# Optimization experiments

Measured on AMD Instinct MI355X. Metric: run time of the kernel, lower is better.

The kernel has to match this reference:

```python
import jax, jax.numpy as jnp
import numpy as np
from jax import lax

BS, NT, CH, K = 8, 128, 1024, 4
H = 512  # num_output_chanls // 2 per direction (bidirectional)
G = 4 * H  # gate dim, PyTorch order i,f,g,o


def setup_inputs() -> dict:
    key = jax.random.key(0)
    ks = jax.random.split(key, 9)
    s = 1.0 / np.sqrt(H)
    u = lambda k_, shape: jax.random.uniform(k_, shape, jnp.float32, -s, s)
    return {
        "inputs": jax.random.normal(ks[0], (BS, NT, CH, K), jnp.float32),
        "Wih_f": u(ks[1], (K, G, CH)),
        "Whh_f": u(ks[2], (K, G, H)),
        "bih_f": u(ks[3], (K, G)),
        "bhh_f": u(ks[4], (K, G)),
        "Wih_b": u(ks[5], (K, G, CH)),
        "Whh_b": u(ks[6], (K, G, H)),
        "bih_b": u(ks[7], (K, G)),
        "bhh_b": u(ks[8], (K, G)),
    }


def _lstm_dir(x_tbck, Wih, Whh, bih, bhh, reverse):
    # x_tbck: [nt, bs, ch, k]; weights batched over k heads.
    bs = x_tbck.shape[1]
    k, _, h = Whh.shape
    bias = bih + bhh  # [k, 4h]

    def step(carry, x_t):
        h_prev, c_prev = carry
        # detach_hidden_state=True: hidden state detached each step
        h_prev = lax.stop_gradient(h_prev)
        c_prev = lax.stop_gradient(c_prev)
        gates = (jnp.einsum('bck,kgc->bkg', x_t, Wih)
                 + jnp.einsum('bkh,kgh->bkg', h_prev, Whh)
                 + bias)  # [bs, k, 4h]
        i, f, g, o = jnp.split(gates, 4, axis=-1)
        c_new = jax.nn.sigmoid(f) * c_prev + jax.nn.sigmoid(i) * jnp.tanh(g)
        h_new = jax.nn.sigmoid(o) * jnp.tanh(c_new)
        return (h_new, c_new), h_new

    init = (jnp.zeros((bs, k, h), x_tbck.dtype), jnp.zeros((bs, k, h), x_tbck.dtype))
    _, hs = lax.scan(step, init, x_tbck, reverse=reverse)  # [nt, bs, k, h]
    return hs


def reference(inputs, Wih_f, Whh_f, bih_f, bhh_f, Wih_b, Whh_b, bih_b, bhh_b):
    # inputs: [bs, nt, ch, k] -> scan over time
    x = jnp.transpose(inputs, (1, 0, 2, 3))  # [nt, bs, ch, k]
    hs_f = _lstm_dir(x, Wih_f, Whh_f, bih_f, bhh_f, reverse=False)
    hs_b = _lstm_dir(x, Wih_b, Whh_b, bih_b, bhh_b, reverse=True)
    # [nt, bs, k, h] -> [bs, nt, h, k]; concat forward/backward on hidden dim
    hs_f = jnp.transpose(hs_f, (1, 0, 3, 2))
    hs_b = jnp.transpose(hs_b, (1, 0, 3, 2))
    return jnp.concatenate([hs_f, hs_b], axis=2)  # [bs, nt, 2h, k]
```

## Files before the change

kernel.cpp:

```cpp
#include <hip/hip_runtime.h>
#include <stdint.h>


typedef __attribute__((ext_vector_type(8))) short short8;
typedef __attribute__((ext_vector_type(4))) float floatx4;
typedef unsigned long long ull;

#define POISON 0x7FC07FC07FC07FC0ull

#define LDS_BARRIER()                                       \
  do {                                                      \
    asm volatile("s_waitcnt lgkmcnt(0)" ::: "memory");      \
    __builtin_amdgcn_s_barrier();                           \
  } while (0)

#define GLOAD_LDS16(g, l)                                        \
  __builtin_amdgcn_global_load_lds(                              \
      (const __attribute__((address_space(1))) void*)(g),        \
      (__attribute__((address_space(3))) void*)(l), 16, 0, 0)

__device__ __forceinline__ unsigned short f2bf(float f) {
  unsigned u = __float_as_uint(f);
  u = (u + 0x7fffu + ((u >> 16) & 1u)) >> 16;
  return (unsigned short)u;
}
__device__ __forceinline__ float sigm(float x) { return 1.0f / (1.0f + __expf(-x)); }
__device__ __forceinline__ float tanh_f(float x) {
  float ax = fabsf(x);
  float e = __expf(-2.0f * ax);
  float t = (1.0f - e) / (1.0f + e);
  return x < 0.0f ? -t : t;
}

__global__ __launch_bounds__(256) void prep_k(
    const float* __restrict__ x,
    const float* __restrict__ Wih_f, const float* __restrict__ Wih_b,
    const float* __restrict__ Whh_f, const float* __restrict__ Whh_b,
    unsigned short* __restrict__ Xp, unsigned short* __restrict__ Wihb,
    unsigned short* __restrict__ Whhb, ull* __restrict__ stateS) {
  size_t i = (size_t)blockIdx.x * 256 + threadIdx.x;
  if (i < 1048576) {
    int g = (int)i;
    int m = g >> 10, c = g & 1023;
    int t = m >> 3, b = m & 7;
    float4 v = *(const float4*)(x + ((size_t)((b * 128 + t) * 1024 + c)) * 4);
    Xp[g]           = f2bf(v.x);
    Xp[1048576 + g] = f2bf(v.y);
    Xp[2097152 + g] = f2bf(v.z);
    Xp[3145728 + g] = f2bf(v.w);
  } else if (i < 3145728) {
    size_t j = i - 1048576;
    float4 v = ((const float4*)Wih_f)[j];
    ushort4 o;
    o.x = f2bf(v.x); o.y = f2bf(v.y); o.z = f2bf(v.z); o.w = f2bf(v.w);
    ((ushort4*)Wihb)[j] = o;
  } else if (i < 5242880) {
    size_t j = i - 3145728;
    float4 v = ((const float4*)Wih_b)[j];
    ushort4 o;
    o.x = f2bf(v.x); o.y = f2bf(v.y); o.z = f2bf(v.z); o.w = f2bf(v.w);
    ((ushort4*)Wihb)[2097152 + j] = o;
  } else if (i < 6291456) {
    size_t j = i - 5242880;
    float4 v = ((const float4*)Whh_f)[j];
    ushort4 o;
    o.x = f2bf(v.x); o.y = f2bf(v.y); o.z = f2bf(v.z); o.w = f2bf(v.w);
    ((ushort4*)Whhb)[j] = o;
  } else if (i < 7340032) {
    size_t j = i - 6291456;
    float4 v = ((const float4*)Whh_b)[j];
    ushort4 o;
    o.x = f2bf(v.x); o.y = f2bf(v.y); o.z = f2bf(v.z); o.w = f2bf(v.w);
    ((ushort4*)Whhb)[1048576 + j] = o;
  } else {
    stateS[i - 7340032] = POISON;
  }
}

__global__ __launch_bounds__(256) void gemm_ih_k(
    const unsigned short* __restrict__ Xp, const unsigned short* __restrict__ Wb,
    const float* __restrict__ bihf, const float* __restrict__ bhhf,
    const float* __restrict__ bihb, const float* __restrict__ bhhb,
    float* __restrict__ ih) {
  const int bid = blockIdx.x;
  const int xcd = bid & 7;
  const int q   = bid >> 3;
  const int mt  = q & 7;
  const int p   = (q >> 3) * 8 + xcd;
  const int dk  = p >> 4;
  const int ntl = p & 15;
  const int kh = dk & 3;
  const int tid = threadIdx.x;
  const int L = tid & 63, w = tid >> 6;
  const int wm = w & 1, wn = w >> 1;
  const int quad = L >> 4, lo = L & 15;

  __shared__ unsigned short As[128 * 32];
  __shared__ unsigned short Bs[128 * 32];

  const unsigned short* Ab = Xp + (size_t)kh * 1048576 + (size_t)mt * 128 * 1024;
  const unsigned short* Bb = Wb + (size_t)dk * 2097152 + (size_t)ntl * 128 * 1024;

  floatx4 acc[4][4] = {};

  for (int kc = 0; kc < 32; ++kc) {
#pragma unroll
    for (int ph = 0; ph < 2; ++ph) {
      int c = ph * 256 + w * 64 + L;
      int ldsb = (ph * 256 + w * 64) * 8;
      GLOAD_LDS16(Ab + (size_t)(c >> 2) * 1024 + kc * 32 + (c & 3) * 8, As + ldsb);
      GLOAD_LDS16(Bb + (size_t)(c >> 2) * 1024 + kc * 32 + (c & 3) * 8, Bs + ldsb);
    }
    __syncthreads();
    short8 af[4], bf[4];
#pragma unroll
    for (int mi = 0; mi < 4; ++mi)
      af[mi] = *(const short8*)(As + (wm * 64 + mi * 16 + lo) * 32 + quad * 8);
#pragma unroll
    for (int ni = 0; ni < 4; ++ni)
      bf[ni] = *(const short8*)(Bs + (wn * 64 + ni * 16 + lo) * 32 + quad * 8);
#pragma unroll
    for (int mi = 0; mi < 4; ++mi)
#pragma unroll
      for (int ni = 0; ni < 4; ++ni)
        acc[mi][ni] = __builtin_amdgcn_mfma_f32_16x16x32_bf16(af[mi], bf[ni], acc[mi][ni], 0, 0, 0);
    __syncthreads();
  }

  const float* bihp = (dk < 4) ? bihf : bihb;
  const float* bhhp = (dk < 4) ? bhhf : bhhb;
#pragma unroll
  for (int ni = 0; ni < 4; ++ni) {
    int g = ntl * 128 + wn * 64 + ni * 16 + lo;
    float bv = bihp[kh * 2048 + g] + bhhp[kh * 2048 + g];
#pragma unroll
    for (int mi = 0; mi < 4; ++mi)
#pragma unroll
      for (int r = 0; r < 4; ++r) {
        int m = mt * 128 + wm * 64 + mi * 16 + quad * 4 + r;
        ih[((size_t)dk * 1024 + m) * 2048 + g] = acc[mi][ni][r] + bv;
      }
  }
}

__global__ __launch_bounds__(256) void lstm_rec_k(
    const float* __restrict__ ih, const unsigned short* __restrict__ whh,
    float* __restrict__ out, ull* __restrict__ stateS) {
  const int tid = threadIdx.x;
  const int L = tid & 63;
  const int w = tid >> 6;
  const int grp = blockIdx.x & 7;
  const int d = grp >> 2, kh = grp & 3;
  const int wg = blockIdx.x >> 3;
  const int j0 = wg * 32;
  const int quad = L >> 4, lo = L & 15;

  __shared__ unsigned short h_lds[16 * 520];
  __shared__ float gbuf[4][8][32];

  for (int i = tid; i < 16 * 520; i += 256) h_lds[i] = 0;

  short8 bfrag[2][16];
#pragma unroll
  for (int ni = 0; ni < 2; ++ni) {
    const unsigned short* wb =
        whh + ((size_t)grp * 2048 + (size_t)(w * 512 + j0 + ni * 16 + lo)) * 512 + quad * 8;
#pragma unroll
    for (int kk = 0; kk < 16; ++kk) bfrag[ni][kk] = *(const short8*)(wb + kk * 32);
  }

  const int pb = tid >> 5, pjj = tid & 31;
  float creg = 0.0f;

  float ihv[2][4];
  {
    int t0 = d ? 127 : 0;
#pragma unroll
    for (int ni = 0; ni < 2; ++ni) {
      const float* ihp =
          ih + ((size_t)grp * 1024 + (size_t)t0 * 8) * 2048 + (w * 512 + j0 + ni * 16 + lo);
#pragma unroll
      for (int r = 0; r < 4; ++r) {
        int b = quad * 4 + r;
        ihv[ni][r] = (b < 8) ? ihp[(size_t)b * 2048] : 0.0f;
      }
    }
  }

  const int srow = tid >> 5;
  const int scol = (tid & 31) * 16;

  for (int s = 0; s < 128; ++s) {
    const int t = d ? (127 - s) : s;

    float ihvN[2][4];
    if (s < 127) {
      int tn = d ? (126 - s) : (s + 1);
#pragma unroll
      for (int ni = 0; ni < 2; ++ni) {
        const float* ihp =
            ih + ((size_t)grp * 1024 + (size_t)tn * 8) * 2048 + (w * 512 + j0 + ni * 16 + lo);
#pragma unroll
        for (int r = 0; r < 4; ++r) {
          int b = quad * 4 + r;
          ihvN[ni][r] = (b < 8) ? ihp[(size_t)b * 2048] : 0.0f;
        }
      }
    } else {
#pragma unroll
      for (int ni = 0; ni < 2; ++ni)
#pragma unroll
        for (int r = 0; r < 4; ++r) ihvN[ni][r] = 0.0f;
    }

    if (s) {
      const ull* src = stateS + ((size_t)grp * 128 + s) * 1024 + tid * 4;
      ull v0, v1, v2, v3;
      do {
        v0 = __hip_atomic_load(src + 0, __ATOMIC_RELAXED, __HIP_MEMORY_SCOPE_AGENT);
        v1 = __hip_atomic_load(src + 1, __ATOMIC_RELAXED, __HIP_MEMORY_SCOPE_AGENT);
        v2 = __hip_atomic_load(src + 2, __ATOMIC_RELAXED, __HIP_MEMORY_SCOPE_AGENT);
        v3 = __hip_atomic_load(src + 3, __ATOMIC_RELAXED, __HIP_MEMORY_SCOPE_AGENT);
      } while (v0 == POISON || v1 == POISON || v2 == POISON || v3 == POISON);
      unsigned short* dl = h_lds + srow * 520 + scol;
      *(ull*)(dl + 0) = v0;
      *(ull*)(dl + 4) = v1;
      *(ull*)(dl + 8) = v2;
      *(ull*)(dl + 12) = v3;
    }
    LDS_BARRIER();

    floatx4 acc[2] = {};
    floatx4 acc2[2] = {};
    {
      const unsigned short* ar = h_lds + lo * 520 + quad * 8;
#pragma unroll
      for (int kk = 0; kk < 16; kk += 2) {
        short8 a0 = *(const short8*)(ar + kk * 32);
        short8 a1 = *(const short8*)(ar + (kk + 1) * 32);
#pragma unroll
        for (int ni = 0; ni < 2; ++ni) {
          acc[ni]  = __builtin_amdgcn_mfma_f32_16x16x32_bf16(a0, bfrag[ni][kk], acc[ni], 0, 0, 0);
          acc2[ni] = __builtin_amdgcn_mfma_f32_16x16x32_bf16(a1, bfrag[ni][kk + 1], acc2[ni], 0, 0, 0);
        }
      }
    }
#pragma unroll
    for (int ni = 0; ni < 2; ++ni)
#pragma unroll
      for (int r = 0; r < 4; ++r) {
        int b = quad * 4 + r;
        if (b < 8) gbuf[w][b][ni * 16 + lo] = acc[ni][r] + acc2[ni][r] + ihv[ni][r];
      }
    LDS_BARRIER();

    {
      float ig = gbuf[0][pb][pjj], fg = gbuf[1][pb][pjj];
      float gg = gbuf[2][pb][pjj], og = gbuf[3][pb][pjj];
      float cn = sigm(fg) * creg + sigm(ig) * tanh_f(gg);
      creg = cn;
      float h = sigm(og) * tanh_f(cn);

      if (s < 127) {
        unsigned hs = f2bf(h);
        int base = L & ~3;
        unsigned v0 = __shfl(hs, base + 0);
        unsigned v1 = __shfl(hs, base + 1);
        unsigned v2 = __shfl(hs, base + 2);
        unsigned v3 = __shfl(hs, base + 3);
        if ((L & 3) == 0) {
          ull wv = (ull)v0 | ((ull)v1 << 16) | ((ull)v2 << 32) | ((ull)v3 << 48);
          ull* dst = stateS + ((size_t)grp * 128 + (s + 1)) * 1024 + pb * 128 + ((j0 + pjj) >> 2);
          __hip_atomic_store(dst, wv, __ATOMIC_RELAXED, __HIP_MEMORY_SCOPE_AGENT);
        }
      }
      out[(((size_t)pb * 128 + t) * 1024 + d * 512 + j0 + pjj) * 4 + kh] = h;
    }

#pragma unroll
    for (int ni = 0; ni < 2; ++ni)
#pragma unroll
      for (int r = 0; r < 4; ++r) ihv[ni][r] = ihvN[ni][r];
  }
}

extern "C" void kernel_launch(void* const* d_in, const int* in_sizes, int n_in,
                              void* d_out, int out_size, void* d_ws, size_t ws_size,
                              hipStream_t stream) {
  (void)in_sizes; (void)n_in; (void)out_size; (void)ws_size;
  const float* x     = (const float*)d_in[0];
  const float* Wih_f = (const float*)d_in[1];
  const float* Whh_f = (const float*)d_in[2];
  const float* bih_f = (const float*)d_in[3];
  const float* bhh_f = (const float*)d_in[4];
  const float* Wih_b = (const float*)d_in[5];
  const float* Whh_b = (const float*)d_in[6];
  const float* bih_b = (const float*)d_in[7];
  const float* bhh_b = (const float*)d_in[8];
  float* out = (float*)d_out;
  char* ws = (char*)d_ws;

  ull* stateS          = (ull*)ws;
  float* ihg           = (float*)(ws + (8ull << 20));
  unsigned short* Xp   = (unsigned short*)(ws + (72ull << 20));
  unsigned short* Wihb = (unsigned short*)(ws + (80ull << 20));
  unsigned short* Whhb = (unsigned short*)(ws + (112ull << 20));

  prep_k<<<32768, 256, 0, stream>>>(x, Wih_f, Wih_b, Whh_f, Whh_b, Xp, Wihb, Whhb, stateS);
  gemm_ih_k<<<1024, 256, 0, stream>>>(Xp, Wihb, bih_f, bhh_f, bih_b, bhh_b, ihg);
  lstm_rec_k<<<128, 256, 0, stream>>>(ihg, Whhb, out, stateS);
}
```

Measured before the change: 418.9 us.

## Split input-GEMM: 256x256 tile kernel for first head, vectorize input bf16 pack

Vectorizes the input conversion in prep_k so each thread packs four channels and issues 16-byte loads and 8-byte stores, reducing the thread count. The input-projection GEMM for direction/head 0 is moved to a new 256x256-tile kernel that uses 512 threads, double-buffered direct-to-LDS loads and an XOR-swizzled layout. The remaining 7 direction/head slices stay on the existing 128x128 kernel. This likely aims at a dependency: the recurrence for the first slice could then start earlier or get better reuse. It adds a second GEMM launch, and the large tile yields only 32 blocks for that slice.

```diff
diff --git a/kernel.cpp b/kernel.cpp
--- a/kernel.cpp
+++ b/kernel.cpp
@@ -39,41 +39,49 @@
     unsigned short* __restrict__ Xp, unsigned short* __restrict__ Wihb,
     unsigned short* __restrict__ Whhb, ull* __restrict__ stateS) {
   size_t i = (size_t)blockIdx.x * 256 + threadIdx.x;
-  if (i < 1048576) {
-    int g = (int)i;
-    int m = g >> 10, c = g & 1023;
+  if (i < 262144) {
+    int m = (int)i >> 8, cb = (int)i & 255;
     int t = m >> 3, b = m & 7;
-    float4 v = *(const float4*)(x + ((size_t)((b * 128 + t) * 1024 + c)) * 4);
-    Xp[g]           = f2bf(v.x);
-    Xp[1048576 + g] = f2bf(v.y);
-    Xp[2097152 + g] = f2bf(v.z);
-    Xp[3145728 + g] = f2bf(v.w);
-  } else if (i < 3145728) {
-    size_t j = i - 1048576;
+    const float* xs = x + ((size_t)((b * 128 + t) * 1024 + cb * 4)) * 4;
+    float4 v0 = ((const float4*)xs)[0];
+    float4 v1 = ((const float4*)xs)[1];
+    float4 v2 = ((const float4*)xs)[2];
+    float4 v3 = ((const float4*)xs)[3];
+    int o = m * 1024 + cb * 4;
+    ushort4 o0 = {f2bf(v0.x), f2bf(v1.x), f2bf(v2.x), f2bf(v3.x)};
+    ushort4 o1 = {f2bf(v0.y), f2bf(v1.y), f2bf(v2.y), f2bf(v3.y)};
+    ushort4 o2 = {f2bf(v0.z), f2bf(v1.z), f2bf(v2.z), f2bf(v3.z)};
+    ushort4 o3 = {f2bf(v0.w), f2bf(v1.w), f2bf(v2.w), f2bf(v3.w)};
+    *(ushort4*)(Xp + o)           = o0;
+    *(ushort4*)(Xp + 1048576 + o) = o1;
+    *(ushort4*)(Xp + 2097152 + o) = o2;
+    *(ushort4*)(Xp + 3145728 + o) = o3;
+  } else if (i < 2359296) {
+    size_t j = i - 262144;
     float4 v = ((const float4*)Wih_f)[j];
     ushort4 o;
     o.x = f2bf(v.x); o.y = f2bf(v.y); o.z = f2bf(v.z); o.w = f2bf(v.w);
     ((ushort4*)Wihb)[j] = o;
-  } else if (i < 5242880) {
-    size_t j = i - 3145728;
+  } else if (i < 4456448) {
+    size_t j = i - 2359296;
     float4 v = ((const float4*)Wih_b)[j];
     ushort4 o;
     o.x = f2bf(v.x); o.y = f2bf(v.y); o.z = f2bf(v.z); o.w = f2bf(v.w);
     ((ushort4*)Wihb)[2097152 + j] = o;
-  } else if (i < 6291456) {
-    size_t j = i - 5242880;
+  } else if (i < 5505024) {
+    size_t j = i - 4456448;
     float4 v = ((const float4*)Whh_f)[j];
     ushort4 o;
     o.x = f2bf(v.x); o.y = f2bf(v.y); o.z = f2bf(v.z); o.w = f2bf(v.w);
     ((ushort4*)Whhb)[j] = o;
-  } else if (i < 7340032) {
-    size_t j = i - 6291456;
+  } else if (i < 6553600) {
+    size_t j = i - 5505024;
     float4 v = ((const float4*)Whh_b)[j];
     ushort4 o;
     o.x = f2bf(v.x); o.y = f2bf(v.y); o.z = f2bf(v.z); o.w = f2bf(v.w);
     ((ushort4*)Whhb)[1048576 + j] = o;
   } else {
-    stateS[i - 7340032] = POISON;
+    stateS[i - 6553600] = POISON;
   }
 }
 
@@ -87,7 +95,7 @@
   const int q   = bid >> 3;
   const int mt  = q & 7;
   const int p   = (q >> 3) * 8 + xcd;
-  const int dk  = p >> 4;
+  const int dk  = (p >> 4) + 1;
   const int ntl = p & 15;
   const int kh = dk & 3;
   const int tid = threadIdx.x;
@@ -141,6 +149,85 @@
         ih[((size_t)dk * 1024 + m) * 2048 + g] = acc[mi][ni][r] + bv;
       }
   }
+}
+
+__global__ __launch_bounds__(512, 2) void gemm256_k(
+    const unsigned short* __restrict__ Xp, const unsigned short* __restrict__ Wb,
+    const float* __restrict__ bihf, const float* __restrict__ bhhf,
+    float* __restrict__ ih) {
+  const int mt = blockIdx.x & 3;
+  const int nt = blockIdx.x >> 2;
+  const int tid = threadIdx.x;
+  const int L = tid & 63, w = tid >> 6;
+  const int wm = w >> 2, wn = w & 3;
+  const int quad = L >> 4, lo = L & 15;
+
+  __shared__ unsigned short smem[65536];
+
+  const unsigned short* Ab = Xp + (size_t)mt * 256 * 1024;
+  const unsigned short* Bb = Wb + (size_t)nt * 256 * 1024;
+
+  floatx4 acc[8][4] = {};
+
+#define STAGE256(t, buf)                                                     \
+  do {                                                                       \
+    unsigned short* SA = smem + (buf) * 32768;                               \
+    unsigned short* SB = SA + 16384;                                         \
+    _Pragma("unroll")                                                        \
+    for (int j = 0; j < 4; ++j) {                                            \
+      int c = j * 512 + tid;                                                 \
+      int row = c >> 3;                                                      \
+      int qs = (c & 7) ^ (row & 7);                                          \
+      int ldsb = (j * 512 + w * 64) * 8;     \
+      GLOAD_LDS16(Ab + (size_t)row * 1024 + (t) * 64 + qs * 8, SA + ldsb);   \
+      GLOAD_LDS16(Bb + (size_t)row * 1024 + (t) * 64 + qs * 8, SB + ldsb);   \
+    }                                                                        \
+  } while (0)
+
+  STAGE256(0, 0);
+  __syncthreads();
+
+  for (int t = 0; t < 16; ++t) {
+    if (t < 15) STAGE256(t + 1, (t + 1) & 1);
+    const unsigned short* SA = smem + (t & 1) * 32768;
+    const unsigned short* SB = SA + 16384;
+#pragma unroll
+    for (int kk = 0; kk < 2; ++kk) {
+      short8 af[8], bf[4];
+#pragma unroll
+      for (int mi = 0; mi < 8; ++mi) {
+        int row = wm * 128 + mi * 16 + lo;
+        int slot = (kk * 4 + quad) ^ (row & 7);
+        af[mi] = *(const short8*)(SA + row * 64 + slot * 8);
+      }
+#pragma unroll
+      for (int ni = 0; ni < 4; ++ni) {
+        int row = wn * 64 + ni * 16 + lo;
+        int slot = (kk * 4 + quad) ^ (row & 7);
+        bf[ni] = *(const short8*)(SB + row * 64 + slot * 8);
+      }
+#pragma unroll
+      for (int mi = 0; mi < 8; ++mi)
+#pragma unroll
+        for (int ni = 0; ni < 4; ++ni)
+          acc[mi][ni] = __builtin_amdgcn_mfma_f32_16x16x32_bf16(af[mi], bf[ni], acc[mi][ni], 0, 0, 0);
+    }
+    __syncthreads();
+  }
+
+#pragma unroll
+  for (int ni = 0; ni < 4; ++ni) {
+    int g = nt * 256 + wn * 64 + ni * 16 + lo;
+    float bv = bihf[g] + bhhf[g];
+#pragma unroll
+    for (int mi = 0; mi < 8; ++mi)
+#pragma unroll
+      for (int r = 0; r < 4; ++r) {
+        int m = mt * 256 + wm * 128 + mi * 16 + quad * 4 + r;
+        ih[(size_t)m * 2048 + g] = acc[mi][ni][r] + bv;
+      }
+  }
+#undef STAGE256
 }
 
 __global__ __launch_bounds__(256) void lstm_rec_k(
@@ -306,7 +393,8 @@
   unsigned short* Wihb = (unsigned short*)(ws + (80ull << 20));
   unsigned short* Whhb = (unsigned short*)(ws + (112ull << 20));
 
-  prep_k<<<32768, 256, 0, stream>>>(x, Wih_f, Wih_b, Whh_f, Whh_b, Xp, Wihb, Whhb, stateS);
-  gemm_ih_k<<<1024, 256, 0, stream>>>(Xp, Wihb, bih_f, bhh_f, bih_b, bhh_b, ihg);
+  prep_k<<<29696, 256, 0, stream>>>(x, Wih_f, Wih_b, Whh_f, Whh_b, Xp, Wihb, Whhb, stateS);
+  gemm_ih_k<<<896, 256, 0, stream>>>(Xp, Wihb, bih_f, bhh_f, bih_b, bhh_b, ihg);
+  gemm256_k<<<32, 512, 0, stream>>>(Xp, Wihb, bih_f, bhh_f, ihg);
   lstm_rec_k<<<128, 256, 0, stream>>>(ihg, Whhb, out, stateS);
 }
```

Result: slower. 441.2 us (+5.3%).
